# Performance work log

Measured on AMD Instinct MI355X. Metric: run time of the kernel, lower is better.

Reference implementation:

```python
import jax, jax.numpy as jnp
import numpy as np

N_NODES = 10000
N_EDGES = 256000
H = 128   # n_hidden_feats
P = 64    # n_product_feats
NB = 8    # n_basis
NS = 10   # n_species
RH = 64   # radial MLP hidden width
RC = 5.0  # r_cutoff
AVG = 25.6  # avg_n_neighbors


def _radial(r):
    # Bessel radial basis * polynomial cutoff envelope (p = n_polynomial_cutoff = 5). r: [E,1]
    n = jnp.arange(1, NB + 1, dtype=r.dtype)
    bessel = jnp.sqrt(2.0 / RC) * jnp.sin(n * jnp.pi * r / RC) / r  # [E,NB]
    u = r / RC
    p = 5.0
    env = 1.0 - 0.5 * (p + 1) * (p + 2) * u**p + p * (p + 2) * u**(p + 1) - 0.5 * p * (p + 1) * u**(p + 2)
    env = jnp.where(u < 1.0, env, 0.0)
    return bessel * env


def _mlp(x, Ws):
    for W in Ws[:-1]:
        x = jax.nn.silu(x @ W)
    return x @ Ws[-1]


def _B0(w, A0, A1):
    # correlation-3 symmetric contractions to a scalar target; w: [N,5,P]
    dot = jnp.sum(A1 * A1, axis=-1)  # [N,P]  (rank-1 . rank-1)
    return (w[:, 0] * A0 + w[:, 1] * A0**2 + w[:, 2] * A0**3
            + w[:, 3] * dot + w[:, 4] * A0 * dot)


def _forward(positions, shifts, node_attrs,
             W_embed, Wsc1, Wup0_1, R1_0, R1_1, R1_2, R1_3,
             Wout0_1, Wout1_1, Wp0_1, Wp1_1, Wl0_1, Wl1_1,
             Wsc2, Wup0_2, Wup1_2, R2_0, R2_1, R2_2, R2_3,
             Wout0_2, Wout1_2, Wp0_2, Wl0_2,
             idx_i, idx_j):
    v = positions[idx_i] - positions[idx_j] - shifts                    # [E,3]
    r = jnp.maximum(jnp.linalg.norm(v, axis=-1, keepdims=True), 1e-9)   # [E,1]
    Y1 = v / r                                                          # Cartesian harmonics, l=1
    edge_feats = _radial(r)                                             # [E,NB]

    feats0 = node_attrs @ W_embed                                       # [N,H] scalar node embedding

    # ---- interaction 1: node feats l=0, edge attrs l<=1 -> targets l<=1 ----
    sc0 = jnp.einsum('nk,kch,nc->nh', node_attrs, Wsc1, feats0)         # per-species residual
    h0 = feats0 @ Wup0_1
    w = _mlp(edge_feats, (R1_0, R1_1, R1_2, R1_3)).reshape(-1, 2, H)    # tp weights per edge
    h0j = h0[idx_j]                                                     # [E,H]
    m0 = w[:, 0] * h0j                                                  # 0x0->0
    m1 = (w[:, 1] * h0j)[:, :, None] * Y1[:, None, :]                   # 0x1->1, [E,H,3]
    a0 = jax.ops.segment_sum(m0, idx_i, num_segments=N_NODES) / AVG
    a1 = jax.ops.segment_sum(m1, idx_i, num_segments=N_NODES) / AVG
    A0 = a0 @ Wout0_1                                                   # [N,P]
    A1 = jnp.einsum('nhd,hp->npd', a1, Wout1_1)                         # [N,P,3]

    # ---- product basis 1 (correlation 3, targets l=0 and l=1) ----
    wp0 = jnp.einsum('nk,kqp->nqp', node_attrs, Wp0_1)                  # [N,5,P]
    wp1 = jnp.einsum('nk,kqp->nqp', node_attrs, Wp1_1)                  # [N,4,P]
    B0 = _B0(wp0, A0, A1)
    dot = jnp.sum(A1 * A1, axis=-1)
    B1 = (wp1[:, 0] + wp1[:, 1] * A0 + wp1[:, 2] * A0**2 + wp1[:, 3] * dot)[:, :, None] * A1
    out0 = B0 @ Wl0_1 + sc0                                             # [N,H]
    out1 = jnp.einsum('npd,ph->nhd', B1, Wl1_1)                         # [N,H,3] (sc has no l=1 part)

    # ---- interaction 2: node feats l<=1, targets l<=1; product target l=0 ----
    sc0b = jnp.einsum('nk,kch,nc->nh', node_attrs, Wsc2, out0)
    g0 = out0 @ Wup0_2
    g1 = jnp.einsum('nhd,hg->ngd', out1, Wup1_2)
    w2 = _mlp(edge_feats, (R2_0, R2_1, R2_2, R2_3)).reshape(-1, 5, H)   # 5 tp paths
    g0j = g0[idx_j]
    g1j = g1[idx_j]
    Y1e = Y1[:, None, :]
    m0 = w2[:, 0] * g0j + w2[:, 3] * jnp.sum(g1j * Y1e, axis=-1)        # 0x0->0, 1x1->0 (dot)
    m1 = ((w2[:, 1] * g0j)[:, :, None] * Y1e                             # 0x1->1
          + w2[:, 2][:, :, None] * g1j                                   # 1x0->1
          + w2[:, 4][:, :, None] * jnp.cross(g1j, jnp.broadcast_to(Y1e, g1j.shape)))  # 1x1->1
    a0 = jax.ops.segment_sum(m0, idx_i, num_segments=N_NODES) / AVG
    a1 = jax.ops.segment_sum(m1, idx_i, num_segments=N_NODES) / AVG
    A0 = a0 @ Wout0_2
    A1 = jnp.einsum('nhd,hp->npd', a1, Wout1_2)
    wp0 = jnp.einsum('nk,kqp->nqp', node_attrs, Wp0_2)
    out0b = _B0(wp0, A0, A1) @ Wl0_2 + sc0b                             # [N,H]

    # torch returns [feats[:, :H] per layer]; the first H flattened columns are the scalar block
    return jnp.stack([out0, out0b], axis=0)                             # [2,N,H]


def setup_inputs() -> dict:
    key = jax.random.key(0)
    ks = iter(jax.random.split(key, 40))

    def nrm(shape, fan_in):
        return jax.random.normal(next(ks), shape, dtype=jnp.float32) / np.sqrt(fan_in)

    positions = jax.random.normal(next(ks), (N_NODES, 3), dtype=jnp.float32) * 8.0
    idx_i = jax.random.randint(next(ks), (N_EDGES,), 0, N_NODES)
    idx_j = jax.random.randint(next(ks), (N_EDGES,), 0, N_NODES)
    shifts = jnp.zeros((N_EDGES, 3), jnp.float32)
    species = jax.random.randint(next(ks), (N_NODES,), 0, NS)
    node_attrs = jax.nn.one_hot(species, NS, dtype=jnp.float32)

    return dict(
        positions=positions, shifts=shifts, node_attrs=node_attrs,
        W_embed=nrm((NS, H), NS),
        Wsc1=nrm((NS, H, H), H), Wup0_1=nrm((H, H), H),
        R1_0=nrm((NB, RH), NB), R1_1=nrm((RH, RH), RH), R1_2=nrm((RH, RH), RH), R1_3=nrm((RH, 2 * H), RH),
        Wout0_1=nrm((H, P), H), Wout1_1=nrm((H, P), H),
        Wp0_1=nrm((NS, 5, P), 1.0), Wp1_1=nrm((NS, 4, P), 1.0),
        Wl0_1=nrm((P, H), P), Wl1_1=nrm((P, H), P),
        Wsc2=nrm((NS, H, H), H), Wup0_2=nrm((H, H), H), Wup1_2=nrm((H, H), H),
        R2_0=nrm((NB, RH), NB), R2_1=nrm((RH, RH), RH), R2_2=nrm((RH, RH), RH), R2_3=nrm((RH, 5 * H), RH),
        Wout0_2=nrm((H, P), H), Wout1_2=nrm((H, P), H),
        Wp0_2=nrm((NS, 5, P), 1.0),
        Wl0_2=nrm((P, H), P),
        idx_i=idx_i, idx_j=idx_j,
    )


def reference(positions, shifts, node_attrs,
              W_embed, Wsc1, Wup0_1, R1_0, R1_1, R1_2, R1_3,
              Wout0_1, Wout1_1, Wp0_1, Wp1_1, Wl0_1, Wl1_1,
              Wsc2, Wup0_2, Wup1_2, R2_0, R2_1, R2_2, R2_3,
              Wout0_2, Wout1_2, Wp0_2, Wl0_2,
              idx_i, idx_j):
    return _forward(positions, shifts, node_attrs,
                    W_embed, Wsc1, Wup0_1, R1_0, R1_1, R1_2, R1_3,
                    Wout0_1, Wout1_1, Wp0_1, Wp1_1, Wl0_1, Wl1_1,
                    Wsc2, Wup0_2, Wup1_2, R2_0, R2_1, R2_2, R2_3,
                    Wout0_2, Wout1_2, Wp0_2, Wl0_2,
                    idx_i, idx_j)
```

## Files before the change

### kernel.cpp

```cpp
#include <hip/hip_runtime.h>
#include <math.h>

#define NN 10000
#define NE 256000
#define HD 128
#define PD 64
#define NBASIS 8
#define NSPEC 10
#define RHID 64
#define RCUT 5.0f
#define INV_AVG 0.0390625f
#define PI_F 3.14159265358979f
#define ECAP 12288
#define NACTCAP 8192
#define RSZ 819

__device__ __forceinline__ float silu(float x) {
    return x / (1.0f + expf(-x));
}

__global__ __launch_bounds__(256) void k_initTables(
    const float* __restrict__ na_, const float* __restrict__ We,
    const float* __restrict__ Wsc1, const float* __restrict__ Wup01,
    const float* __restrict__ Wup02, const float* __restrict__ Wsc2,
    int* __restrict__ spec, int* __restrict__ ecnt, int* cnt, int* eTot,
    int* __restrict__ scurG, int* __restrict__ actLst,
    float* __restrict__ sc0s, float* __restrict__ h0s,
    float* __restrict__ g0d, float* __restrict__ sc0bd) {
    __shared__ float ls[HD];
    int b = blockIdx.x;
    if (b < 40) {
        int n = b * 256 + threadIdx.x;
        if (n == 0) { *cnt = 0; *eTot = 0; }
        if (n < NSPEC) scurG[n] = 0;
        if (n < NACTCAP) actLst[n] = -1;
        if (n >= NN) return;
        ecnt[n] = 0;
        int s = 0;
        for (int k = 0; k < NSPEC; k++)
            if (na_[n * NSPEC + k] > 0.5f) s = k;
        spec[n] = s;
    } else {
        int s = b - 40;
        int t = threadIdx.x;
        if (t < HD) {
            float acc1 = 0.f, acc2 = 0.f;
            for (int c = 0; c < HD; c++) {
                float fe = We[s * HD + c];
                acc1 += fe * Wsc1[((size_t)s * HD + c) * HD + t];
                acc2 += fe * Wup01[c * HD + t];
            }
            sc0s[s * HD + t] = acc1;
            h0s[s * HD + t] = acc2;
            ls[t] = acc1;
        }
        __syncthreads();
        if (t < HD) {
            float a1 = 0.f, a2 = 0.f;
            for (int c = 0; c < HD; c++) {
                float v = ls[c];
                a1 += v * Wup02[c * HD + t];
                a2 += v * Wsc2[((size_t)s * HD + c) * HD + t];
            }
            g0d[s * HD + t] = a1;
            sc0bd[s * HD + t] = a2;
        }
    }
}

__global__ __launch_bounds__(256) void k_compact(
    const float* __restrict__ pos, const float* __restrict__ shifts,
    const int* __restrict__ ii, const int* __restrict__ jj,
    int* cnt, int* __restrict__ ecnt,
    int* __restrict__ ui, int* __restrict__ uj,
    float* __restrict__ uY, float* __restrict__ uF) {
    __shared__ int lTot;
    __shared__ int blockBase;
    int t = threadIdx.x;
    if (t == 0) lTot = 0;
    __syncthreads();
    int e0 = (blockIdx.x * 256 + t) * 4;
    int iv[4], jv[4], keep[4];
    float vx[4], vy[4], vz[4], rr[4];
    #pragma unroll
    for (int k = 0; k < 4; k++) {
        int e = e0 + k;
        int i = ii[e], j = jj[e];
        iv[k] = i; jv[k] = j;
        float x = pos[i * 3 + 0] - pos[j * 3 + 0] - shifts[e * 3 + 0];
        float y = pos[i * 3 + 1] - pos[j * 3 + 1] - shifts[e * 3 + 1];
        float z = pos[i * 3 + 2] - pos[j * 3 + 2] - shifts[e * 3 + 2];
        float r = sqrtf(x * x + y * y + z * z);
        r = fmaxf(r, 1e-9f);
        vx[k] = x; vy[k] = y; vz[k] = z; rr[k] = r;
        keep[k] = (r < RCUT) ? 1 : 0;
    }
    int myCnt = keep[0] + keep[1] + keep[2] + keep[3];
    int myOff = 0;
    if (myCnt) myOff = atomicAdd(&lTot, myCnt);
    __syncthreads();
    if (t == 0) blockBase = atomicAdd(cnt, lTot);
    __syncthreads();
    int slot = blockBase + myOff;
    #pragma unroll
    for (int k = 0; k < 4; k++) {
        if (!keep[k]) continue;
        int i = iv[k];
        atomicAdd(&ecnt[i], 1);
        ui[slot] = i; uj[slot] = jv[k];
        float r = rr[k];
        float inv = 1.0f / r;
        uY[slot * 3 + 0] = vx[k] * inv;
        uY[slot * 3 + 1] = vy[k] * inv;
        uY[slot * 3 + 2] = vz[k] * inv;
        float u = r * (1.0f / RCUT);
        float u5 = u * u * u * u * u;
        float env = 1.0f - 21.0f * u5 + 35.0f * u5 * u - 15.0f * u5 * u * u;
        float c0 = 0.6324555320336759f * env * inv;
        float th = PI_F * u;
        float s1, c1;
        __sincosf(th, &s1, &c1);
        float two_c1 = 2.0f * c1;
        float sp = 0.f, sn = s1;
        uF[slot * NBASIS + 0] = c0 * sn;
        #pragma unroll
        for (int b = 1; b < NBASIS; b++) {
            float s_new = two_c1 * sn - sp;
            sp = sn; sn = s_new;
            uF[slot * NBASIS + b] = c0 * sn;
        }
        slot++;
    }
}

__global__ __launch_bounds__(256) void k_assignPlace(
    const int* __restrict__ ecnt, const int* __restrict__ spec,
    int* __restrict__ ebase, int* __restrict__ ecur,
    int* eTot, int* scurG,
    int* __restrict__ actIndex, int* __restrict__ actList) {
    __shared__ int lTot;
    __shared__ int blockBase;
    __shared__ int lHist[NSPEC];
    __shared__ int lBase[NSPEC];
    int t = threadIdx.x;
    int n = blockIdx.x * 256 + t;
    if (t == 0) lTot = 0;
    if (t < NSPEC) lHist[t] = 0;
    __syncthreads();
    int ec = (n < NN) ? ecnt[n] : 0;
    int s = (n < NN) ? spec[n] : 0;
    bool act = (ec > 0);
    int myOff = 0, myIdx = 0;
    if (act) {
        myOff = atomicAdd(&lTot, ec);
        myIdx = atomicAdd(&lHist[s], 1);
    }
    __syncthreads();
    if (t == 0) blockBase = atomicAdd(eTot, lTot);
    if (t < NSPEC) lBase[t] = (lHist[t] > 0) ? atomicAdd(&scurG[t], lHist[t]) : 0;
    __syncthreads();
    if (n < NN) {
        if (act) {
            int b = blockBase + myOff;
            ebase[n] = b;
            ecur[n] = b;
            int rank = lBase[s] + myIdx;
            if (rank < RSZ) {
                int p = s * RSZ + rank;
                actList[p] = n;
                actIndex[n] = p;
            } else {
                actIndex[n] = -1;
            }
        } else {
            actIndex[n] = -1;
        }
    }
}

__global__ __launch_bounds__(256) void k_sortFill(
    const int* cnt, const int* __restrict__ ui, const int* __restrict__ uj,
    const float* __restrict__ uY, const float* __restrict__ uF,
    int* __restrict__ ecur, int* __restrict__ sj,
    float* __restrict__ sY, float* __restrict__ sF,
    const int* __restrict__ spec, const float* __restrict__ sc0s,
    const float* __restrict__ sc0bd,
    float* __restrict__ out0g, float* __restrict__ outbg) {
    int b = blockIdx.x;
    if (b < 48) {
        int e = b * 256 + threadIdx.x;
        int n = *cnt; if (n > ECAP) n = ECAP;
        if (e >= n) return;
        int slot = atomicAdd(&ecur[ui[e]], 1);
        if (slot >= ECAP) return;
        sj[slot] = uj[e];
        #pragma unroll
        for (int d = 0; d < 3; d++) sY[slot * 3 + d] = uY[e * 3 + d];
        #pragma unroll
        for (int bb = 0; bb < NBASIS; bb++) sF[slot * NBASIS + bb] = uF[e * NBASIS + bb];
    } else {
        int t = (b - 48) * 256 + threadIdx.x;
        int n = t >> 6, c = t & 63;
        if (n >= NN) return;
        int s = spec[n];
        out0g[(size_t)n * HD + c] = sc0s[s * HD + c];
        out0g[(size_t)n * HD + 64 + c] = sc0s[s * HD + 64 + c];
        outbg[(size_t)n * HD + c] = sc0bd[s * HD + c];
        outbg[(size_t)n * HD + 64 + c] = sc0bd[s * HD + 64 + c];
    }
}

__global__ __launch_bounds__(256) void k_hid(
    const int* cnt, const float* __restrict__ sF,
    const float* __restrict__ A0, const float* __restrict__ A1, const float* __restrict__ A2,
    const float* __restrict__ B0, const float* __restrict__ B1, const float* __restrict__ B2,
    float* __restrict__ xh1, float* __restrict__ xh2) {
    int lane = threadIdx.x & 63;
    int wid = (blockIdx.x * 256 + threadIdx.x) >> 6;
    int ne = *cnt; if (ne > ECAP) ne = ECAP;
    int base = wid * 2;
    if (base >= ne) return;
    const float* W0 = (blockIdx.y == 0) ? A0 : B0;
    const float* W1 = (blockIdx.y == 0) ? A1 : B1;
    const float* W2 = (blockIdx.y == 0) ? A2 : B2;
    float* dst = (blockIdx.y == 0) ? xh1 : xh2;
    int e0 = base, e1 = (base + 1 < ne) ? base + 1 : base;
    float x0, x1;
    {
        float F0[NBASIS], F1[NBASIS];
        #pragma unroll
        for (int b = 0; b < NBASIS; b++) { F0[b] = sF[e0 * NBASIS + b]; F1[b] = sF[e1 * NBASIS + b]; }
        float a0 = 0.f, a1 = 0.f;
        #pragma unroll
        for (int b = 0; b < NBASIS; b++) {
            float wv = W0[b * RHID + lane];
            a0 += F0[b] * wv; a1 += F1[b] * wv;
        }
        x0 = silu(a0); x1 = silu(a1);
    }
    {
        float c0 = 0.f, c1 = 0.f;
        for (int c = 0; c < RHID; c++) {
            float wv = W1[c * RHID + lane];
            c0 += __shfl(x0, c) * wv; c1 += __shfl(x1, c) * wv;
        }
        x0 = silu(c0); x1 = silu(c1);
    }
    {
        float c0 = 0.f, c1 = 0.f;
        for (int c = 0; c < RHID; c++) {
            float wv = W2[c * RHID + lane];
            c0 += __shfl(x0, c) * wv; c1 += __shfl(x1, c) * wv;
        }
        x0 = silu(c0); x1 = silu(c1);
    }
    dst[(size_t)e0 * RHID + lane] = x0;
    if (base + 1 < ne) dst[(size_t)e1 * RHID + lane] = x1;
}

__global__ __launch_bounds__(256) void k_wmat(
    const int* cnt, const float* __restrict__ xh1, const float* __restrict__ xh2,
    const float* __restrict__ A3, const float* __restrict__ B3,
    float* __restrict__ ew1, float* __restrict__ ew2) {
    __shared__ float sX[64 * 65];
    int t = threadIdx.x;
    int ne = *cnt; if (ne > ECAP) ne = ECAP;
    int y = blockIdx.y;
    int eBase = blockIdx.x * 64;
    if (eBase >= ne) return;
    const float* X; const float* W; float* dst; int ncol, col0;
    if (y < 2) { X = xh1; W = A3; dst = ew1; ncol = 2 * HD; col0 = y * 128; }
    else       { X = xh2; W = B3; dst = ew2; ncol = 5 * HD; col0 = (y - 2) * 128; }
    {
        const float4* src = (const float4*)(X + (size_t)eBase * RHID);
        #pragma unroll
        for (int it = 0; it < 4; it++) {
            int idx = t + it * 256;
            float4 v = src[idx];
            int e = idx >> 4, c4 = (idx & 15) * 4;
            float* d = &sX[e * 65 + c4];
            d[0] = v.x; d[1] = v.y; d[2] = v.z; d[3] = v.w;
        }
    }
    __syncthreads();
    int sgrp = t >> 4;
    int cg = col0 + (t & 15) * 8;
    float acc[4][8] = {};
    for (int c = 0; c < RHID; c++) {
        float xk[4];
        #pragma unroll
        for (int k = 0; k < 4; k++) xk[k] = sX[(sgrp * 4 + k) * 65 + c];
        float4 wA = *(const float4*)(W + (size_t)c * ncol + cg);
        float4 wB = *(const float4*)(W + (size_t)c * ncol + cg + 4);
        float wv[8] = {wA.x, wA.y, wA.z, wA.w, wB.x, wB.y, wB.z, wB.w};
        #pragma unroll
        for (int k = 0; k < 4; k++)
            #pragma unroll
            for (int q = 0; q < 8; q++)
                acc[k][q] += xk[k] * wv[q];
    }
    #pragma unroll
    for (int k = 0; k < 4; k++) {
        int e = eBase + sgrp * 4 + k;
        *(float4*)(dst + (size_t)e * ncol + cg) =
            make_float4(acc[k][0], acc[k][1], acc[k][2], acc[k][3]);
        *(float4*)(dst + (size_t)e * ncol + cg + 4) =
            make_float4(acc[k][4], acc[k][5], acc[k][6], acc[k][7]);
    }
}

__global__ __launch_bounds__(256) void k_agg1(
    const int* __restrict__ actList,
    const int* __restrict__ ebase, const int* __restrict__ ecnt,
    const int* __restrict__ sj, const float* __restrict__ sY,
    const float* __restrict__ ew, const int* __restrict__ spec,
    const float* __restrict__ h0s, float* __restrict__ a0c, float* __restrict__ a1c) {
    int lane = threadIdx.x & 63;
    int ia = (blockIdx.x * 256 + threadIdx.x) >> 6;
    int h = blockIdx.y * 64;
    int n = actList[ia];
    if (n < 0) return;
    int eb = ebase[n], ec = ecnt[n];
    float a0 = 0.f;
    float a1[3] = {0,0,0};
    for (int idx = eb; idx < eb + ec; idx++) {
        int j = sj[idx];
        int sp = spec[j];
        float h0 = h0s[sp * HD + h + lane];
        const float* w = ew + (size_t)idx * 256;
        float w0 = w[h + lane], w1 = w[128 + h + lane];
        a0 += w0 * h0;
        float m1 = w1 * h0;
        #pragma unroll
        for (int d = 0; d < 3; d++) a1[d] += m1 * sY[idx * 3 + d];
    }
    a0c[(size_t)ia * HD + h + lane] = a0 * INV_AVG;
    #pragma unroll
    for (int d = 0; d < 3; d++)
        a1c[((size_t)d * NACTCAP + ia) * HD + h + lane] = a1[d] * INV_AVG;
}

__global__ __launch_bounds__(256) void k_proj(
    const int* __restrict__ actList,
    const float* __restrict__ x0buf, const float* __restrict__ x1buf,
    const float* __restrict__ W0, const float* __restrict__ W1,
    float* __restrict__ am0, float* __restrict__ am1) {
    __shared__ float sX[16 * HD];
    int lane = threadIdx.x & 63;
    int w = __builtin_amdgcn_readfirstlane((int)(threadIdx.x >> 6));
    int y = blockIdx.y;
    const float* X = (y == 0) ? x0buf : (x1buf + (size_t)(y - 1) * NACTCAP * HD);
    const float* W = (y == 0) ? W0 : W1;
    int iaBase = blockIdx.x * 16;
    {
        const float4* src = (const float4*)(X + (size_t)iaBase * HD);
        float4* d4 = (float4*)sX;
        #pragma unroll
        for (int it = 0; it < 2; it++)
            d4[threadIdx.x + it * 256] = src[threadIdx.x + it * 256];
    }
    __syncthreads();
    bool any = false;
    int ia0 = iaBase + w * 4;
    #pragma unroll
    for (int k = 0; k < 4; k++) any = any || (actList[ia0 + k] >= 0);
    if (!any) return;
    float* dst = (y == 0) ? am0 : (am1 + (size_t)(y - 1) * NACTCAP * PD);
    int w4 = w * 4;
    float acc[4] = {0,0,0,0};
    for (int c = 0; c < HD; c += 4) {
        float4 xv[4];
        #pragma unroll
        for (int k = 0; k < 4; k++) xv[k] = *(const float4*)&sX[(w4 + k) * HD + c];
        #pragma unroll
        for (int cc = 0; cc < 4; cc++) {
            float wv = W[(c + cc) * PD + lane];
            #pragma unroll
            for (int k = 0; k < 4; k++) {
                float xc = (cc==0)?xv[k].x:(cc==1)?xv[k].y:(cc==2)?xv[k].z:xv[k].w;
                acc[k] += xc * wv;
            }
        }
    }
    #pragma unroll
    for (int k = 0; k < 4; k++) dst[(size_t)(ia0 + k) * PD + lane] = acc[k];
}

__global__ __launch_bounds__(256) void k_bout(
    const int* __restrict__ actList,
    const float* __restrict__ am0, const float* __restrict__ am1,
    const int* __restrict__ spec,
    const float* __restrict__ Wp0, const float* __restrict__ Wp1,
    const float* __restrict__ Wl0, const float* __restrict__ Wl1,
    const float* __restrict__ sc0s,
    float* __restrict__ out0g, float* __restrict__ out0c, float* __restrict__ out1c) {
    __shared__ float sB[4][8][PD];
    int lane = threadIdx.x & 63;
    int w = __builtin_amdgcn_readfirstlane((int)(threadIdx.x >> 6));
    int y = blockIdx.y;
    int bs = y >> 1, h = (y & 1) * 64;
    int ia0 = (blockIdx.x * 4 + w) * 8;
    int nv[8], sk[8];
    bool any = false;
    #pragma unroll
    for (int k = 0; k < 8; k++) {
        nv[k] = actList[ia0 + k];
        any = any || (nv[k] >= 0);
        sk[k] = spec[(nv[k] >= 0) ? nv[k] : 0];
    }
    if (!any) return;
    #pragma unroll
    for (int k = 0; k < 8; k++) {
        int ia = ia0 + k;
        int s = sk[k];
        float A0v = am0[(size_t)ia * PD + lane];
        float a1x = am1[((size_t)0 * NACTCAP + ia) * PD + lane];
        float a1y = am1[((size_t)1 * NACTCAP + ia) * PD + lane];
        float a1z = am1[((size_t)2 * NACTCAP + ia) * PD + lane];
        float dot = a1x * a1x + a1y * a1y + a1z * a1z;
        float A02 = A0v * A0v;
        float B;
        if (bs == 0) {
            const float* wp = Wp0 + (size_t)(s * 5) * PD;
            B = wp[lane] * A0v + wp[PD + lane] * A02 + wp[2 * PD + lane] * A02 * A0v +
                wp[3 * PD + lane] * dot + wp[4 * PD + lane] * A0v * dot;
        } else {
            const float* wp = Wp1 + (size_t)(s * 4) * PD;
            float fac = wp[lane] + wp[PD + lane] * A0v + wp[2 * PD + lane] * A02 + wp[3 * PD + lane] * dot;
            float a1d = (bs == 1) ? a1x : ((bs == 2) ? a1y : a1z);
            B = fac * a1d;
        }
        sB[w][k][lane] = B;
    }
    const float* Wl = (bs == 0) ? Wl0 : Wl1;
    float o[8] = {0,0,0,0,0,0,0,0};
    for (int q = 0; q < PD; q += 4) {
        float4 bq[8];
        #pragma unroll
        for (int k = 0; k < 8; k++) bq[k] = *(const float4*)&sB[w][k][q];
        #pragma unroll
        for (int qq = 0; qq < 4; qq++) {
            float wl = Wl[(q + qq) * HD + h + lane];
            #pragma unroll
            for (int k = 0; k < 8; k++) {
                float b = (qq==0)?bq[k].x:(qq==1)?bq[k].y:(qq==2)?bq[k].z:bq[k].w;
                o[k] += b * wl;
            }
        }
    }
    if (bs == 0) {
        #pragma unroll
        for (int k = 0; k < 8; k++) {
            int ia = ia0 + k;
            float v = o[k] + sc0s[sk[k] * HD + h + lane];
            if (nv[k] >= 0) out0g[(size_t)nv[k] * HD + h + lane] = v;
            out0c[(size_t)ia * HD + h + lane] = v;
        }
    } else {
        float* dst = out1c + (size_t)(bs - 1) * NACTCAP * HD;
        #pragma unroll
        for (int k = 0; k < 8; k++)
            dst[(size_t)(ia0 + k) * HD + h + lane] = o[k];
    }
}

__global__ __launch_bounds__(256) void k_g(
    const int* __restrict__ actList, const int* __restrict__ spec,
    const float* __restrict__ out0c, const float* __restrict__ out1c,
    const float* __restrict__ Wsc2, const float* __restrict__ Wup02, const float* __restrict__ Wup12,
    float* __restrict__ sc0bc, float* __restrict__ g0c, float* __restrict__ g1c) {
    __shared__ float sX[64 * 129];
    __shared__ int sSpec[64];
    __shared__ int sB0, sAny, sMis;
    int t = threadIdx.x;
    int st = blockIdx.y;
    int slotBase = blockIdx.x * 64;
    const float* X = (st <= 1) ? out0c : (out1c + (size_t)(st - 2) * NACTCAP * HD);
    if (t < 64) {
        int n = actList[slotBase + t];
        sSpec[t] = (n >= 0) ? spec[n] : -1;
    }
    __syncthreads();
    if (t == 0) {
        int sb = 0, any = 0, mis = 0;
        for (int k = 0; k < 64; k++) {
            int sv = sSpec[k];
            if (sv >= 0) {
                if (!any) { sb = sv; any = 1; }
                else if (sv != sb) mis = 1;
            }
        }
        sB0 = sb; sAny = any; sMis = mis;
    }
    __syncthreads();
    if (!sAny) return;
    {
        const float4* src = (const float4*)(X + (size_t)slotBase * HD);
        #pragma unroll
        for (int it = 0; it < 8; it++) {
            int idx = t + it * 256;
            float4 v = src[idx];
            int e = idx >> 5, c4 = (idx & 31) * 4;
            float* d = &sX[e * 129 + c4];
            d[0] = v.x; d[1] = v.y; d[2] = v.z; d[3] = v.w;
        }
    }
    __syncthreads();
    const float* Wt = (st == 0) ? (Wsc2 + (size_t)sB0 * HD * HD)
                    : ((st == 1) ? Wup02 : Wup12);
    float* dst = (st == 0) ? sc0bc : ((st == 1) ? g0c : (g1c + (size_t)(st - 2) * NACTCAP * HD));
    int sgrp = t >> 4;
    int cg = (t & 15) * 8;
    float acc[4][8] = {};
    for (int c = 0; c < HD; c++) {
        float xk[4];
        #pragma unroll
        for (int k = 0; k < 4; k++) xk[k] = sX[(sgrp * 4 + k) * 129 + c];
        float4 wA = *(const float4*)(Wt + (size_t)c * HD + cg);
        float4 wB = *(const float4*)(Wt + (size_t)c * HD + cg + 4);
        float wv[8] = {wA.x, wA.y, wA.z, wA.w, wB.x, wB.y, wB.z, wB.w};
        #pragma unroll
        for (int k = 0; k < 4; k++)
            #pragma unroll
            for (int q = 0; q < 8; q++)
                acc[k][q] += xk[k] * wv[q];
    }
    #pragma unroll
    for (int k = 0; k < 4; k++) {
        int slot = slotBase + sgrp * 4 + k;
        *(float4*)(dst + (size_t)slot * HD + cg) =
            make_float4(acc[k][0], acc[k][1], acc[k][2], acc[k][3]);
        *(float4*)(dst + (size_t)slot * HD + cg + 4) =
            make_float4(acc[k][4], acc[k][5], acc[k][6], acc[k][7]);
    }
    if (st == 0 && sMis) {
        __syncthreads();
        for (int k = 0; k < 64; k++) {
            int sv = sSpec[k];
            if (sv < 0 || sv == sB0) continue;
            if (t < HD) {
                const float* Wm = Wsc2 + (size_t)sv * HD * HD;
                float p = 0.f;
                for (int c = 0; c < HD; c++) p += sX[k * 129 + c] * Wm[c * HD + t];
                sc0bc[(size_t)(slotBase + k) * HD + t] = p;
            }
        }
    }
}

__global__ __launch_bounds__(256) void k_agg2(
    const int* __restrict__ actList,
    const int* __restrict__ ebase, const int* __restrict__ ecnt,
    const int* __restrict__ sj, const float* __restrict__ sY,
    const float* __restrict__ ew, const int* __restrict__ spec,
    const int* __restrict__ actIndex,
    const float* __restrict__ g0c, const float* __restrict__ g1c,
    const float* __restrict__ g0d,
    float* __restrict__ a0c, float* __restrict__ a1c) {
    int lane = threadIdx.x & 63;
    int ia = (blockIdx.x * 256 + threadIdx.x) >> 6;
    int h = blockIdx.y * 64;
    int n = actList[ia];
    if (n < 0) return;
    int eb = ebase[n], ec = ecnt[n];
    float m0 = 0.f;
    float s1[3] = {0,0,0};
    for (int idx = eb; idx < eb + ec; idx++) {
        int j = sj[idx];
        float Yx = sY[idx * 3 + 0], Yy = sY[idx * 3 + 1], Yz = sY[idx * 3 + 2];
        int ji = actIndex[j];
        float gv, gx, gy, gz;
        if (ji >= 0) {
            gv = g0c[(size_t)ji * HD + h + lane];
            gx = g1c[((size_t)0 * NACTCAP + ji) * HD + h + lane];
            gy = g1c[((size_t)1 * NACTCAP + ji) * HD + h + lane];
            gz = g1c[((size_t)2 * NACTCAP + ji) * HD + h + lane];
        } else {
            gv = g0d[spec[j] * HD + h + lane];
            gx = gy = gz = 0.f;
        }
        const float* wr = ew + (size_t)idx * 640;
        float w0 = wr[h + lane];
        float w1 = wr[128 + h + lane];
        float w2 = wr[256 + h + lane];
        float w3 = wr[384 + h + lane];
        float w4 = wr[512 + h + lane];
        float dot = gx * Yx + gy * Yy + gz * Yz;
        m0 += w0 * gv + w3 * dot;
        float cx = gy * Yz - gz * Yy, cy = gz * Yx - gx * Yz, cz = gx * Yy - gy * Yx;
        s1[0] += w1 * gv * Yx + w2 * gx + w4 * cx;
        s1[1] += w1 * gv * Yy + w2 * gy + w4 * cy;
        s1[2] += w1 * gv * Yz + w2 * gz + w4 * cz;
    }
    a0c[(size_t)ia * HD + h + lane] = m0 * INV_AVG;
    #pragma unroll
    for (int d = 0; d < 3; d++)
        a1c[((size_t)d * NACTCAP + ia) * HD + h + lane] = s1[d] * INV_AVG;
}

__global__ __launch_bounds__(256) void k_outC(
    const int* __restrict__ actList, const int* __restrict__ spec,
    const float* __restrict__ am0, const float* __restrict__ am1,
    const float* __restrict__ Wp0, const float* __restrict__ Wl0,
    const float* __restrict__ sc0bc, float* __restrict__ outbg) {
    __shared__ float sB[4][8][PD];
    int lane = threadIdx.x & 63;
    int w = __builtin_amdgcn_readfirstlane((int)(threadIdx.x >> 6));
    int h = blockIdx.y * 64;
    int ia0 = (blockIdx.x * 4 + w) * 8;
    int nv[8];
    bool any = false;
    #pragma unroll
    for (int k = 0; k < 8; k++) { nv[k] = actList[ia0 + k]; any = any || (nv[k] >= 0); }
    if (!any) return;
    #pragma unroll
    for (int k = 0; k < 8; k++) {
        int ia = ia0 + k;
        int s = spec[(nv[k] >= 0) ? nv[k] : 0];
        float A0v = am0[(size_t)ia * PD + lane];
        float a1x = am1[((size_t)0 * NACTCAP + ia) * PD + lane];
        float a1y = am1[((size_t)1 * NACTCAP + ia) * PD + lane];
        float a1z = am1[((size_t)2 * NACTCAP + ia) * PD + lane];
        float dot = a1x * a1x + a1y * a1y + a1z * a1z;
        float A02 = A0v * A0v;
        const float* wp = Wp0 + (size_t)(s * 5) * PD;
        sB[w][k][lane] = wp[lane] * A0v + wp[PD + lane] * A02 + wp[2 * PD + lane] * A02 * A0v +
                         wp[3 * PD + lane] * dot + wp[4 * PD + lane] * A0v * dot;
    }
    float o[8] = {0,0,0,0,0,0,0,0};
    for (int q = 0; q < PD; q += 4) {
        float4 bq[8];
        #pragma unroll
        for (int k = 0; k < 8; k++) bq[k] = *(const float4*)&sB[w][k][q];
        #pragma unroll
        for (int qq = 0; qq < 4; qq++) {
            float wl = Wl0[(q + qq) * HD + h + lane];
            #pragma unroll
            for (int k = 0; k < 8; k++) {
                float b = (qq==0)?bq[k].x:(qq==1)?bq[k].y:(qq==2)?bq[k].z:bq[k].w;
                o[k] += b * wl;
            }
        }
    }
    #pragma unroll
    for (int k = 0; k < 8; k++) {
        if (nv[k] < 0) continue;
        int ia = ia0 + k;
        outbg[(size_t)nv[k] * HD + h + lane] = o[k] + sc0bc[(size_t)ia * HD + h + lane];
    }
}

extern "C" void kernel_launch(void* const* d_in, const int* in_sizes, int n_in,
                              void* d_out, int out_size, void* d_ws, size_t ws_size,
                              hipStream_t stream) {
    const float* pos    = (const float*)d_in[0];
    const float* shifts = (const float*)d_in[1];
    const float* na     = (const float*)d_in[2];
    const float* We     = (const float*)d_in[3];
    const float* Wsc1   = (const float*)d_in[4];
    const float* Wup01  = (const float*)d_in[5];
    const float* R10    = (const float*)d_in[6];
    const float* R11    = (const float*)d_in[7];
    const float* R12    = (const float*)d_in[8];
    const float* R13    = (const float*)d_in[9];
    const float* Wout01 = (const float*)d_in[10];
    const float* Wout11 = (const float*)d_in[11];
    const float* Wp01   = (const float*)d_in[12];
    const float* Wp11   = (const float*)d_in[13];
    const float* Wl01   = (const float*)d_in[14];
    const float* Wl11   = (const float*)d_in[15];
    const float* Wsc2   = (const float*)d_in[16];
    const float* Wup02  = (const float*)d_in[17];
    const float* Wup12  = (const float*)d_in[18];
    const float* R20    = (const float*)d_in[19];
    const float* R21    = (const float*)d_in[20];
    const float* R22    = (const float*)d_in[21];
    const float* R23    = (const float*)d_in[22];
    const float* Wout02 = (const float*)d_in[23];
    const float* Wout12 = (const float*)d_in[24];
    const float* Wp02   = (const float*)d_in[25];
    const float* Wl02   = (const float*)d_in[26];
    const int*   idx_i  = (const int*)d_in[27];
    const int*   idx_j  = (const int*)d_in[28];
    float* out = (float*)d_out;
    float* outb = out + (size_t)NN * HD;

    char* ws = (char*)d_ws;
    size_t off = 0;
    auto alloc = [&](size_t bytes) -> char* {
        char* pp = ws + off;
        off += (bytes + 255) & ~(size_t)255;
        return pp;
    };
    int*   cnt    = (int*)alloc(4);
    int*   eTot   = (int*)alloc(4);
    int*   scurG  = (int*)alloc(NSPEC * 4);
    int*   spec   = (int*)alloc((size_t)NN * 4);
    int*   ecnt   = (int*)alloc((size_t)NN * 4);
    int*   ebase  = (int*)alloc((size_t)NN * 4);
    int*   ecur   = (int*)alloc((size_t)NN * 4);
    int*   actIdx = (int*)alloc((size_t)NN * 4);
    int*   actLst = (int*)alloc((size_t)NACTCAP * 4);
    float* sc0s   = (float*)alloc((size_t)NSPEC * HD * 4);
    float* h0s    = (float*)alloc((size_t)NSPEC * HD * 4);
    float* g0d    = (float*)alloc((size_t)NSPEC * HD * 4);
    float* sc0bd  = (float*)alloc((size_t)NSPEC * HD * 4);
    int*   sj     = (int*)alloc((size_t)ECAP * 4);
    float* sYv    = (float*)alloc((size_t)ECAP * 3 * 4);
    float* sFv    = (float*)alloc((size_t)ECAP * NBASIS * 4);
    float* xh1    = (float*)alloc((size_t)ECAP * RHID * 4);
    float* xh2    = (float*)alloc((size_t)ECAP * RHID * 4);
    float* ew1    = (float*)alloc((size_t)ECAP * 256 * 4);
    float* ew2    = (float*)alloc((size_t)ECAP * 640 * 4);
    int*   ui     = (int*)ew2;
    int*   uj     = ui + NE;
    float* uY     = (float*)(uj + NE);
    float* uF     = uY + (size_t)NE * 3;
    float* a0c    = (float*)alloc((size_t)NACTCAP * HD * 4);
    float* a1c    = (float*)alloc((size_t)NACTCAP * HD * 3 * 4);
    float* am0    = (float*)alloc((size_t)NACTCAP * PD * 4);
    float* am1    = (float*)alloc((size_t)NACTCAP * PD * 3 * 4);
    float* out0c  = (float*)alloc((size_t)NACTCAP * HD * 4);
    float* out1c  = (float*)alloc((size_t)NACTCAP * HD * 3 * 4);
    float* g0c    = (float*)alloc((size_t)NACTCAP * HD * 4);
    float* g1c    = (float*)alloc((size_t)NACTCAP * HD * 3 * 4);
    float* sc0bc  = (float*)alloc((size_t)NACTCAP * HD * 4);

    k_initTables<<<50, 256, 0, stream>>>(na, We, Wsc1, Wup01, Wup02, Wsc2,
                                         spec, ecnt, cnt, eTot, scurG, actLst,
                                         sc0s, h0s, g0d, sc0bd);
    k_compact<<<NE / 1024, 256, 0, stream>>>(pos, shifts, idx_i, idx_j, cnt, ecnt,
                                             ui, uj, uY, uF);
    k_assignPlace<<<(NN + 255) / 256, 256, 0, stream>>>(ecnt, spec, ebase, ecur,
                                                        eTot, scurG, actIdx, actLst);
    k_sortFill<<<48 + (NN * 64) / 256, 256, 0, stream>>>(cnt, ui, uj, uY, uF, ecur,
                                                         sj, sYv, sFv,
                                                         spec, sc0s, sc0bd, out, outb);
    k_hid<<<dim3(ECAP / 8, 2), 256, 0, stream>>>(cnt, sFv, R10, R11, R12,
                                                 R20, R21, R22, xh1, xh2);
    k_wmat<<<dim3(ECAP / 64, 7), 256, 0, stream>>>(cnt, xh1, xh2, R13, R23, ew1, ew2);
    k_agg1<<<dim3(NACTCAP / 4, 2), 256, 0, stream>>>(actLst, ebase, ecnt, sj, sYv, ew1,
                                                     spec, h0s, a0c, a1c);
    k_proj<<<dim3(NACTCAP / 16, 4), 256, 0, stream>>>(actLst, a0c, a1c, Wout01, Wout11,
                                                      am0, am1);
    k_bout<<<dim3(NACTCAP / 32, 8), 256, 0, stream>>>(actLst, am0, am1, spec,
                                                      Wp01, Wp11, Wl01, Wl11, sc0s,
                                                      out, out0c, out1c);
    k_g<<<dim3(NACTCAP / 64, 5), 256, 0, stream>>>(actLst, spec, out0c, out1c,
                                                   Wsc2, Wup02, Wup12, sc0bc, g0c, g1c);
    k_agg2<<<dim3(NACTCAP / 4, 2), 256, 0, stream>>>(actLst, ebase, ecnt, sj, sYv, ew2,
                                                     spec, actIdx, g0c, g1c, g0d, a0c, a1c);
    k_proj<<<dim3(NACTCAP / 16, 4), 256, 0, stream>>>(actLst, a0c, a1c, Wout02, Wout12,
                                                      am0, am1);
    k_outC<<<dim3(NACTCAP / 32, 2), 256, 0, stream>>>(actLst, spec, am0, am1, Wp02, Wl02,
                                                      sc0bc, outb);
}
```

Measured before the change: 176.8 us.

## Tile radial MLP hidden layers with shared-memory 4x4 register blocking

Rewrites the radial-MLP hidden-layer kernel so each block handles 64 edges. Basis features and intermediate activations are staged in padded shared memory, and each thread computes a 4-edge by 4-column register tile using float4 weight loads. This replaces the per-wave two-edge loop with shuffles, cutting redundant weight loads and shuffle traffic. In exchange it adds block-wide barriers and uses about 35KB of shared memory per block, which may limit occupancy.

```diff
diff --git a/kernel.cpp b/kernel.cpp
--- a/kernel.cpp
+++ b/kernel.cpp
@@ -215,47 +215,93 @@
     const float* __restrict__ A0, const float* __restrict__ A1, const float* __restrict__ A2,
     const float* __restrict__ B0, const float* __restrict__ B1, const float* __restrict__ B2,
     float* __restrict__ xh1, float* __restrict__ xh2) {
-    int lane = threadIdx.x & 63;
-    int wid = (blockIdx.x * 256 + threadIdx.x) >> 6;
+    __shared__ float sf[64 * 9];
+    __shared__ float xA[64 * 65];
+    __shared__ float xB[64 * 65];
+    int t = threadIdx.x;
     int ne = *cnt; if (ne > ECAP) ne = ECAP;
-    int base = wid * 2;
-    if (base >= ne) return;
+    int eBase = blockIdx.x * 64;
+    if (eBase >= ne) return;
     const float* W0 = (blockIdx.y == 0) ? A0 : B0;
     const float* W1 = (blockIdx.y == 0) ? A1 : B1;
     const float* W2 = (blockIdx.y == 0) ? A2 : B2;
     float* dst = (blockIdx.y == 0) ? xh1 : xh2;
-    int e0 = base, e1 = (base + 1 < ne) ? base + 1 : base;
-    float x0, x1;
+    if (t < 128) {
+        float4 v = *(const float4*)(sF + (size_t)eBase * NBASIS + t * 4);
+        int e = t >> 1, c = (t & 1) * 4;
+        float* d = &sf[e * 9 + c];
+        d[0] = v.x; d[1] = v.y; d[2] = v.z; d[3] = v.w;
+    }
+    __syncthreads();
+    int sgrp = t >> 4;
+    int cg = (t & 15) * 4;
     {
-        float F0[NBASIS], F1[NBASIS];
-        #pragma unroll
-        for (int b = 0; b < NBASIS; b++) { F0[b] = sF[e0 * NBASIS + b]; F1[b] = sF[e1 * NBASIS + b]; }
-        float a0 = 0.f, a1 = 0.f;
-        #pragma unroll
-        for (int b = 0; b < NBASIS; b++) {
-            float wv = W0[b * RHID + lane];
-            a0 += F0[b] * wv; a1 += F1[b] * wv;
-        }
-        x0 = silu(a0); x1 = silu(a1);
-    }
+        float acc[4][4] = {};
+        #pragma unroll
+        for (int c = 0; c < NBASIS; c++) {
+            float xk[4];
+            #pragma unroll
+            for (int k = 0; k < 4; k++) xk[k] = sf[(sgrp * 4 + k) * 9 + c];
+            float4 wv = *(const float4*)(W0 + c * RHID + cg);
+            float wq[4] = {wv.x, wv.y, wv.z, wv.w};
+            #pragma unroll
+            for (int k = 0; k < 4; k++)
+                #pragma unroll
+                for (int q = 0; q < 4; q++)
+                    acc[k][q] += xk[k] * wq[q];
+        }
+        #pragma unroll
+        for (int k = 0; k < 4; k++)
+            #pragma unroll
+            for (int q = 0; q < 4; q++)
+                xA[(sgrp * 4 + k) * 65 + cg + q] = silu(acc[k][q]);
+    }
+    __syncthreads();
     {
-        float c0 = 0.f, c1 = 0.f;
+        float acc[4][4] = {};
         for (int c = 0; c < RHID; c++) {
-            float wv = W1[c * RHID + lane];
-            c0 += __shfl(x0, c) * wv; c1 += __shfl(x1, c) * wv;
-        }
-        x0 = silu(c0); x1 = silu(c1);
-    }
+            float xk[4];
+            #pragma unroll
+            for (int k = 0; k < 4; k++) xk[k] = xA[(sgrp * 4 + k) * 65 + c];
+            float4 wv = *(const float4*)(W1 + c * RHID + cg);
+            float wq[4] = {wv.x, wv.y, wv.z, wv.w};
+            #pragma unroll
+            for (int k = 0; k < 4; k++)
+                #pragma unroll
+                for (int q = 0; q < 4; q++)
+                    acc[k][q] += xk[k] * wq[q];
+        }
+        #pragma unroll
+        for (int k = 0; k < 4; k++)
+            #pragma unroll
+            for (int q = 0; q < 4; q++)
+                xB[(sgrp * 4 + k) * 65 + cg + q] = silu(acc[k][q]);
+    }
+    __syncthreads();
     {
-        float c0 = 0.f, c1 = 0.f;
+        float acc[4][4] = {};
         for (int c = 0; c < RHID; c++) {
-            float wv = W2[c * RHID + lane];
-            c0 += __shfl(x0, c) * wv; c1 += __shfl(x1, c) * wv;
-        }
-        x0 = silu(c0); x1 = silu(c1);
-    }
-    dst[(size_t)e0 * RHID + lane] = x0;
-    if (base + 1 < ne) dst[(size_t)e1 * RHID + lane] = x1;
+            float xk[4];
+            #pragma unroll
+            for (int k = 0; k < 4; k++) xk[k] = xB[(sgrp * 4 + k) * 65 + c];
+            float4 wv = *(const float4*)(W2 + c * RHID + cg);
+            float wq[4] = {wv.x, wv.y, wv.z, wv.w};
+            #pragma unroll
+            for (int k = 0; k < 4; k++)
+                #pragma unroll
+                for (int q = 0; q < 4; q++)
+                    acc[k][q] += xk[k] * wq[q];
+        }
+        #pragma unroll
+        for (int k = 0; k < 4; k++) {
+            int e = eBase + sgrp * 4 + k;
+            if (e < ne) {
+                *(float4*)(dst + (size_t)e * RHID + cg) =
+                    make_float4(silu(acc[k][0]), silu(acc[k][1]),
+                                silu(acc[k][2]), silu(acc[k][3]));
+            }
+        }
+    }
 }
 
 __global__ __launch_bounds__(256) void k_wmat(
@@ -736,8 +782,8 @@
     k_sortFill<<<48 + (NN * 64) / 256, 256, 0, stream>>>(cnt, ui, uj, uY, uF, ecur,
                                                          sj, sYv, sFv,
                                                          spec, sc0s, sc0bd, out, outb);
-    k_hid<<<dim3(ECAP / 8, 2), 256, 0, stream>>>(cnt, sFv, R10, R11, R12,
-                                                 R20, R21, R22, xh1, xh2);
+    k_hid<<<dim3(ECAP / 64, 2), 256, 0, stream>>>(cnt, sFv, R10, R11, R12,
+                                                  R20, R21, R22, xh1, xh2);
     k_wmat<<<dim3(ECAP / 64, 7), 256, 0, stream>>>(cnt, xh1, xh2, R13, R23, ew1, ew2);
     k_agg1<<<dim3(NACTCAP / 4, 2), 256, 0, stream>>>(actLst, ebase, ecnt, sj, sYv, ew1,
                                                      spec, h0s, a0c, a1c);
```

After: 172.6 us (median of 2 runs). -2.3%, faster.
